# Kernel tuning notes

Hardware: AMD Instinct MI355X
Metric: run time of the kernel (lower is better)

The kernel has to match this reference:

```python
import jax, jax.numpy as jnp
import numpy as np

B, D, G, L = 8, 128, 2048, 24
GF = G // 2 + 1  # rfft bins
EPS = 1e-5


def setup_inputs() -> dict:
    key = jax.random.key(0)
    ks = jax.random.split(key, 6)
    x = jax.random.normal(ks[0], (B, D, G), dtype=jnp.float32)
    Phi_f = jax.random.normal(ks[1], (L, GF), dtype=jnp.float32) * 0.1
    Theta = jax.random.normal(ks[2], (L, D, D), dtype=jnp.float32) * (1.0 / np.sqrt(D))
    ln_gamma = jnp.ones((D,), dtype=jnp.float32)
    ln_beta = jnp.zeros((D,), dtype=jnp.float32)
    fc1_w = jax.random.normal(ks[3], (2 * D, D), dtype=jnp.float32) * (1.0 / np.sqrt(D))
    fc1_b = jnp.zeros((2 * D,), dtype=jnp.float32)
    fc2_w = jax.random.normal(ks[4], (D, 2 * D), dtype=jnp.float32) * (1.0 / np.sqrt(2 * D))
    fc2_b = jnp.zeros((D,), dtype=jnp.float32)
    return {
        'x': x, 'Phi_f': Phi_f, 'Theta': Theta,
        'ln_gamma': ln_gamma, 'ln_beta': ln_beta,
        'fc1_w': fc1_w, 'fc1_b': fc1_b, 'fc2_w': fc2_w, 'fc2_b': fc2_b,
    }


def reference(x, Phi_f, Theta, ln_gamma, ln_beta, fc1_w, fc1_b, fc2_w, fc2_b):
    # x: (B, D, G). LayerNorm over the lifting (channel) dim D.
    mean = jnp.mean(x, axis=1, keepdims=True)
    var = jnp.var(x, axis=1, keepdims=True)
    z = (x - mean) * jax.lax.rsqrt(var + EPS)
    z = z * ln_gamma[None, :, None] + ln_beta[None, :, None]

    # Spectral convolution with each Hilbert filter.
    Xf = jnp.fft.rfft(z, axis=-1)                       # (B, D, GF) complex
    Uf = Xf[:, :, None, :] * jnp.conj(Phi_f)[None, None]  # (B, D, L, GF)
    U = jnp.fft.irfft(Uf, n=G, axis=-1)                 # (B, D, L, G)

    # Per-filter channel mixing then reduction over filters:
    # einsum('bdln,lhd->bhln') followed by sum over l, fused:
    S = jnp.einsum('bdlg,lhd->bhg', U, Theta)           # (B, D, G)

    # Pointwise MLP (Conv1d kernel_size=1 == channel matmul).
    H = jnp.einsum('hd,bdg->bhg', fc1_w, S) + fc1_b[None, :, None]
    H = jax.nn.gelu(H, approximate=False)
    out = jnp.einsum('dh,bhg->bdg', fc2_w, H) + fc2_b[None, :, None]
    return x + out
```

## Files before the change

kernel.cpp:

```cpp
#include <hip/hip_runtime.h>
#include <math.h>


#define B_   8
#define D_   128
#define G_   2048
#define L_   24
#define GF_  1025
#define BD_  1024
#define DD_  16384
#define GQ_  512
#define MC_  512
#define NF4_ 4096

#define PA_CV0 256
#define PA_TT0 322
#define PA_WF0 578
#define PA_WI0 1090
#define PA_END 1602

#define G1_NB  512
#define G1_END 4736

typedef __attribute__((ext_vector_type(8))) short  short8v;
typedef __attribute__((ext_vector_type(4))) float  float4v;

union FU { float f; unsigned int u; };
union V8 { short8v v; ushort u[8]; };
union V4 { uint2 p; ushort u[4]; };

static __device__ __forceinline__ float bf2f(ushort h) {
    FU v; v.u = ((unsigned int)h) << 16; return v.f;
}
static __device__ __forceinline__ ushort f2bf(float f) {
    FU v; v.f = f;
    unsigned int r = v.u + 0x7fffu + ((v.u >> 16) & 1u);
    return (ushort)(r >> 16);
}
static __device__ __forceinline__ void async16(const void* g, void* l) {
    __builtin_amdgcn_global_load_lds(
        (const __attribute__((address_space(1))) void*)g,
        (__attribute__((address_space(3))) void*)l, 16, 0, 0);
}
static __device__ __forceinline__ int is_f32(const unsigned int* graw) {
    return graw[0] == 0x3F800000u;
}
static __device__ __forceinline__ void crow_inv(int c, int& f, int& im) {
    if (c == 0) { f = 0; im = 0; }
    else        { f = (c + 1) >> 1; im = (c + 1) & 1; }
}

__global__ __launch_bounds__(256) void k_pre(
        const void* __restrict__ x_raw,  const void* __restrict__ th_raw,
        const unsigned int* __restrict__ graw, const void* __restrict__ be_raw,
        const void* __restrict__ w1_raw, const void* __restrict__ b1_raw,
        const void* __restrict__ w2_raw, const void* __restrict__ b2_raw,
        ushort* __restrict__ z,  ushort* __restrict__ wf,
        ushort* __restrict__ wi, ushort* __restrict__ thT,
        ushort* __restrict__ w1c, ushort* __restrict__ b1c,
        ushort* __restrict__ w2c, ushort* __restrict__ b2c) {
    __shared__ ushort T[L_][72];
    __shared__ float red[2][256];
    __shared__ float mi[2][64];
    int bid = blockIdx.x, tid = threadIdx.x;

    if (bid < PA_CV0) {
        int fl = is_f32(graw);
        int b  = bid >> 5;
        int g0 = (bid & 31) * 64;
        int gi = tid & 63, dq = tid >> 6;
        int g  = g0 + gi;
        int d0 = dq * 32;
        float vals[32];
        float s = 0.f, ss = 0.f;
        if (fl) {
            const float* xp = (const float*)x_raw + (size_t)(b * D_ + d0) * G_ + g;
            #pragma unroll 8
            for (int d = 0; d < 32; ++d) {
                float v = xp[(size_t)d * G_];
                vals[d] = v; s += v; ss += v * v;
            }
        } else {
            const ushort* xp = (const ushort*)x_raw + (size_t)(b * D_ + d0) * G_ + g;
            #pragma unroll 8
            for (int d = 0; d < 32; ++d) {
                float v = bf2f(xp[(size_t)d * G_]);
                vals[d] = v; s += v; ss += v * v;
            }
        }
        red[0][tid] = s; red[1][tid] = ss;
        __syncthreads();
        if (tid < 64) {
            float S  = red[0][tid] + red[0][tid + 64] + red[0][tid + 128] +
                       red[0][tid + 192];
            float SS = red[1][tid] + red[1][tid + 64] + red[1][tid + 128] +
                       red[1][tid + 192];
            float mean = S * (1.f / D_);
            float var  = SS * (1.f / D_) - mean * mean;
            mi[0][tid] = mean;
            mi[1][tid] = rsqrtf(var + 1e-5f);
        }
        __syncthreads();
        float mean = mi[0][gi], inv = mi[1][gi];
        ushort* zp = z + (size_t)(g & 3) * (BD_ * GQ_) +
                     (size_t)(b * D_ + d0) * GQ_ + (g >> 2);
        if (fl) {
            const float* gp = (const float*)graw + d0;
            const float* bp = (const float*)be_raw + d0;
            #pragma unroll 8
            for (int d = 0; d < 32; ++d) {
                float o = (vals[d] - mean) * inv * gp[d] + bp[d];
                zp[(size_t)d * GQ_] = f2bf(o);
            }
        } else {
            const ushort* gp = (const ushort*)graw + d0;
            const ushort* bp = (const ushort*)be_raw + d0;
            #pragma unroll 8
            for (int d = 0; d < 32; ++d) {
                float o = (vals[d] - mean) * inv * bf2f(gp[d]) + bf2f(bp[d]);
                zp[(size_t)d * GQ_] = f2bf(o);
            }
        }
    } else if (bid < PA_TT0) {
        int fl = is_f32(graw);
        int lb = bid - PA_CV0;
        const void* src; ushort* dst; int n, rel;
        if (lb < 32)       { src = w1_raw; dst = w1c; n = 32768; rel = lb; }
        else if (lb == 32) { src = b1_raw; dst = b1c; n = 256;   rel = 0; }
        else if (lb < 65)  { src = w2_raw; dst = w2c; n = 32768; rel = lb - 33; }
        else               { src = b2_raw; dst = b2c; n = 128;   rel = 0; }
        int i0 = rel * 1024 + tid * 4;
        if (fl) {
            const float* s = (const float*)src;
            #pragma unroll
            for (int j = 0; j < 4; ++j) {
                int k = i0 + j;
                if (k < n) dst[k] = f2bf(s[k]);
            }
        } else {
            const ushort* s = (const ushort*)src;
            #pragma unroll
            for (int j = 0; j < 4; ++j) {
                int k = i0 + j;
                if (k < n) dst[k] = s[k];
            }
        }
    } else if (bid < PA_WF0) {
        int fl = is_f32(graw);
        int hd0 = (bid - PA_TT0) * 64;
        if (tid < 192) {
            int l = tid >> 3, c8 = tid & 7;
            V8 o;
            if (fl) {
                const float* tp = (const float*)th_raw + (size_t)l * DD_ +
                                  hd0 + c8 * 8;
                float4v a0 = *(const float4v*)tp;
                float4v a1 = *(const float4v*)(tp + 4);
                #pragma unroll
                for (int j = 0; j < 4; ++j) {
                    o.u[j] = f2bf(a0[j]); o.u[4 + j] = f2bf(a1[j]);
                }
            } else {
                o.v = *(const short8v*)((const ushort*)th_raw +
                                        (size_t)l * DD_ + hd0 + c8 * 8);
            }
            *(short8v*)&T[l][c8 * 8] = o.v;
        }
        __syncthreads();
        int hdl = tid & 63, part = tid >> 6;
        V8 o;
        #pragma unroll
        for (int j = 0; j < 8; ++j) {
            int l = part * 8 + j;
            o.u[j] = (l < L_) ? T[l][hdl] : (ushort)0;
        }
        *(short8v*)(thT + (size_t)(hd0 + hdl) * 32 + part * 8) = o.v;
    } else if (bid < PA_WI0) {
        int c = bid - PA_WF0;
        if (tid < 128) {
            int f, im; crow_inv(c, f, im);
            int g0 = tid * 4;
            V4 v;
            #pragma unroll
            for (int j = 0; j < 4; ++j) {
                int g = g0 + j;
                int r = (f * g) & (GQ_ - 1);
                float th = (float)r * 1.2271846303085130e-2f;
                v.u[j] = f2bf(im ? -__sinf(th) : __cosf(th));
            }
            *(uint2*)(wf + (size_t)c * GQ_ + g0) = v.p;
        }
    } else {
        int g = bid - PA_WI0;
        for (int ch = tid; ch < MC_ / 8; ch += 256) {
            int c0 = ch * 8;
            V8 v;
            #pragma unroll
            for (int j = 0; j < 8; ++j) {
                int c = c0 + j;
                int f, im; crow_inv(c, f, im);
                float a = (f == 0 || f == GQ_ / 2) ? 4.8828125e-4f
                                                   : 9.765625e-4f;
                int r = (f * g) & (GQ_ - 1);
                float th = (float)r * 1.2271846303085130e-2f;
                v.u[j] = f2bf(im ? -a * __sinf(th) : a * __cosf(th));
            }
            *(short8v*)(wi + (size_t)g * MC_ + c0) = v.v;
        }
    }
}

__global__ __launch_bounds__(256, 4) void k_g1(
        const ushort* __restrict__ wf, const ushort* __restrict__ z,
        ushort* __restrict__ zft,
        const void* __restrict__ phi_raw, const unsigned int* __restrict__ graw,
        const ushort* __restrict__ thT, ushort* __restrict__ M) {
    __shared__ ushort As[2][64 * 64];
    __shared__ ushort Bs[2][64 * 64];
    __shared__ ushort Aph[16][40];
    int bid = blockIdx.x, tid = threadIdx.x;
    int w = tid >> 6, lane = tid & 63;
    int lr = lane & 15, q = lane >> 4;

    if (bid < G1_NB) {
        int m0 = (bid >> 6) * 64;
        int n0 = (bid & 63) * 64;
        int wm = (w & 1) * 32, wn = (w >> 1) * 32;
        int rl = lane >> 3, c8 = (lane & 7) ^ rl;
        int t0 = w * 2, t1 = w * 2 + 1;
        const ushort* gA0 = wf + (size_t)(m0 + t0 * 8 + rl) * GQ_ + c8 * 8;
        const ushort* gA1 = wf + (size_t)(m0 + t1 * 8 + rl) * GQ_ + c8 * 8;
        const ushort* gB0 = z  + (size_t)(n0 + t0 * 8 + rl) * GQ_ + c8 * 8;
        const ushort* gB1 = z  + (size_t)(n0 + t1 * 8 + rl) * GQ_ + c8 * 8;

        float4v acc00 = {0.f,0.f,0.f,0.f}, acc01 = {0.f,0.f,0.f,0.f};
        float4v acc10 = {0.f,0.f,0.f,0.f}, acc11 = {0.f,0.f,0.f,0.f};

        async16(gA0, &As[0][t0 * 512]);
        async16(gA1, &As[0][t1 * 512]);
        async16(gB0, &Bs[0][t0 * 512]);
        async16(gB1, &Bs[0][t1 * 512]);
        __syncthreads();

        int buf = 0;
        for (int k0 = 0; k0 < GQ_; k0 += 64) {
            if (k0 + 64 < GQ_) {
                int nb = buf ^ 1;
                async16(gA0 + k0 + 64, &As[nb][t0 * 512]);
                async16(gA1 + k0 + 64, &As[nb][t1 * 512]);
                async16(gB0 + k0 + 64, &Bs[nb][t0 * 512]);
                async16(gB1 + k0 + 64, &Bs[nb][t1 * 512]);
            }
            const ushort* Ab = &As[buf][0];
            const ushort* Bb = &Bs[buf][0];
            #pragma unroll
            for (int s = 0; s < 2; ++s) {
                int cs = s * 4 + q;
                int ra0 = wm + lr, ra1 = wm + 16 + lr;
                int rb0 = wn + lr, rb1 = wn + 16 + lr;
                short8v a0 = *(const short8v*)(Ab + ra0 * 64 + ((cs ^ (ra0 & 7)) << 3));
                short8v a1 = *(const short8v*)(Ab + ra1 * 64 + ((cs ^ (ra1 & 7)) << 3));
                short8v b0 = *(const short8v*)(Bb + rb0 * 64 + ((cs ^ (rb0 & 7)) << 3));
                short8v b1 = *(const short8v*)(Bb + rb1 * 64 + ((cs ^ (rb1 & 7)) << 3));
                acc00 = __builtin_amdgcn_mfma_f32_16x16x32_bf16(a0, b0, acc00, 0, 0, 0);
                acc01 = __builtin_amdgcn_mfma_f32_16x16x32_bf16(a0, b1, acc01, 0, 0, 0);
                acc10 = __builtin_amdgcn_mfma_f32_16x16x32_bf16(a1, b0, acc10, 0, 0, 0);
                acc11 = __builtin_amdgcn_mfma_f32_16x16x32_bf16(a1, b1, acc11, 0, 0, 0);
            }
            __syncthreads();
            buf ^= 1;
        }

        float4v accs[2][2] = { { acc00, acc01 }, { acc10, acc11 } };
        #pragma unroll
        for (int i = 0; i < 2; ++i)
            #pragma unroll
            for (int j = 0; j < 2; ++j) {
                int col = n0 + wn + j * 16 + lr;
                int row = m0 + wm + i * 16 + q * 4;
                #pragma unroll
                for (int r = 0; r < 4; ++r)
                    zft[(size_t)(row + r) * NF4_ + col] = f2bf(accs[i][j][r]);
            }
    } else {
        int bb  = bid - G1_NB;
        int f0  = (bb >> 6) * 16;
        int hd0 = (bb & 63) * 256;
        int isf = is_f32(graw);
        #pragma unroll
        for (int rep = 0; rep < 2; ++rep) {
            int idx = rep * 256 + tid;
            int fl = idx >> 5, l = idx & 31;
            int f = f0 + fl;
            ushort v = 0;
            if (l < L_ && f < GF_)
                v = isf ? f2bf(((const float*)phi_raw)[(size_t)l * GF_ + f])
                        : ((const ushort*)phi_raw)[(size_t)l * GF_ + f];
            Aph[fl][l] = v;
        }
        __syncthreads();
        short8v a = *(const short8v*)&Aph[lr][q * 8];
        #pragma unroll
        for (int t = 0; t < 4; ++t) {
            int n = hd0 + (w * 4 + t) * 16 + lr;
            short8v b = *(const short8v*)(thT + (size_t)n * 32 + q * 8);
            float4v c = {0.f, 0.f, 0.f, 0.f};
            c = __builtin_amdgcn_mfma_f32_16x16x32_bf16(a, b, c, 0, 0, 0);
            #pragma unroll
            for (int r = 0; r < 4; ++r) {
                int f = f0 + q * 4 + r;
                if (f < GF_) M[(size_t)f * DD_ + n] = f2bf(c[r]);
            }
        }
    }
}

__global__ __launch_bounds__(256, 2) void k_mix3(const ushort* __restrict__ zft,
                                                 const ushort* __restrict__ M,
                                                 ushort* __restrict__ sft) {
    int bx  = blockIdx.x;
    int fp  = bx >> 1;
    int hh  = bx & 1;
    int tid = threadIdx.x;
    int w = tid >> 6, lane = tid & 63;
    int lr = lane & 15, q = lane >> 4;
    int cc = lr >> 3, bb = lr & 7;
    int ntg = hh * 4 + w;

    int rowRe  = (fp == 0) ? 0 : (fp == 256 ? 511 : 2 * fp - 1);
    int rowIm  = (fp == 0 || fp == 256) ? rowRe : 2 * fp;
    bool has_im = (fp != 0) && (fp != 256);

    float a1 = (float)fp * 3.0679615757712823e-3f;
    float C1 = cosf(a1),        S1 = sinf(a1);
    float C2 = cosf(2.f * a1),  S2 = sinf(2.f * a1);
    float C3 = cosf(3.f * a1),  S3 = sinf(3.f * a1);

    float P01 = cc ? -S1 :  C1,  Q01 = cc ?  C1 :  S1;
    float P02 = cc ? -S2 :  C2,  Q02 = cc ?  C2 :  S2;
    float P03 = cc ? -S3 :  C3,  Q03 = cc ?  C3 :  S3;
    float P11 = cc ? -C1 :  S1,  Q11 = cc ? -S1 : -C1;
    float P12 = cc ? -S2 : -C2,  Q12 = cc ?  C2 : -S2;
    float P13 = cc ?  C3 : -S3,  Q13 = cc ?  S3 :  C3;
    float P21 = cc ? -C1 : -S1,  Q21 = cc ? -S1 :  C1;
    float P22 = cc ?  S2 : -C2,  Q22 = cc ? -C2 : -S2;
    float P23 = cc ?  C3 :  S3,  Q23 = cc ?  S3 : -C3;
    float P31 = cc ? -S1 : -C1,  Q31 = cc ?  C1 : -S1;
    float P32 = cc ?  S2 :  C2,  Q32 = cc ? -C2 :  S2;
    float P33 = cc ? -S3 : -C3,  Q33 = cc ?  C3 : -S3;

    const ushort* r0 = zft + (size_t)rowRe * NF4_;
    const ushort* r1 = zft + (size_t)rowIm * NF4_;
    int colb = bb * 128 + q * 8;

    short8v aZ[4][4];
    #pragma unroll
    for (int s = 0; s < 4; ++s) {
        int col = colb + s * 32;
        V8 R0, I0, R1, I1, R2, I2, R3, I3;
        R0.v = *(const short8v*)(r0 + col);
        I0.v = *(const short8v*)(r1 + col);
        R1.v = *(const short8v*)(r0 + 1024 + col);
        I1.v = *(const short8v*)(r1 + 1024 + col);
        R2.v = *(const short8v*)(r0 + 2048 + col);
        I2.v = *(const short8v*)(r1 + 2048 + col);
        R3.v = *(const short8v*)(r0 + 3072 + col);
        I3.v = *(const short8v*)(r1 + 3072 + col);
        if (!has_im) {
            #pragma unroll
            for (int e = 0; e < 8; ++e) {
                I0.u[e] = 0; I1.u[e] = 0; I2.u[e] = 0; I3.u[e] = 0;
            }
        }
        V8 t0, t1, t2, t3;
        #pragma unroll
        for (int e = 0; e < 8; ++e) {
            float x0 = bf2f(R0.u[e]), y0 = bf2f(I0.u[e]);
            float x1 = bf2f(R1.u[e]), y1 = bf2f(I1.u[e]);
            float x2 = bf2f(R2.u[e]), y2 = bf2f(I2.u[e]);
            float x3 = bf2f(R3.u[e]), y3 = bf2f(I3.u[e]);
            float e0p = cc ?  y0 : x0;
            float e0m = cc ? -y0 : x0;
            float z0 = e0p, z1 = e0m, z2 = e0p, z3 = e0m;
            z0 = fmaf(P01, x1, z0); z0 = fmaf(Q01, y1, z0);
            z0 = fmaf(P02, x2, z0); z0 = fmaf(Q02, y2, z0);
            z0 = fmaf(P03, x3, z0); z0 = fmaf(Q03, y3, z0);
            z1 = fmaf(P11, x1, z1); z1 = fmaf(Q11, y1, z1);
            z1 = fmaf(P12, x2, z1); z1 = fmaf(Q12, y2, z1);
            z1 = fmaf(P13, x3, z1); z1 = fmaf(Q13, y3, z1);
            z2 = fmaf(P21, x1, z2); z2 = fmaf(Q21, y1, z2);
            z2 = fmaf(P22, x2, z2); z2 = fmaf(Q22, y2, z2);
            z2 = fmaf(P23, x3, z2); z2 = fmaf(Q23, y3, z2);
            z3 = fmaf(P31, x1, z3); z3 = fmaf(Q31, y1, z3);
            z3 = fmaf(P32, x2, z3); z3 = fmaf(Q32, y2, z3);
            z3 = fmaf(P33, x3, z3); z3 = fmaf(Q33, y3, z3);
            t0.u[e] = f2bf(z0); t1.u[e] = f2bf(z1);
            t2.u[e] = f2bf(z2); t3.u[e] = f2bf(z3);
        }
        aZ[0][s] = t0.v; aZ[1][s] = t1.v; aZ[2][s] = t2.v; aZ[3][s] = t3.v;
    }

    int fk0 = fp, fk1 = 512 - fp, fk2 = 512 + fp, fk3 = 1024 - fp;
    const ushort* Mp[4] = { M + (size_t)fk0 * DD_, M + (size_t)fk1 * DD_,
                            M + (size_t)fk2 * DD_, M + (size_t)fk3 * DD_ };
    float4v acc[4];
    #pragma unroll
    for (int k = 0; k < 4; ++k) {
        float4v c = {0.f, 0.f, 0.f, 0.f};
        #pragma unroll
        for (int s = 0; s < 4; ++s) {
            short8v bfr = *(const short8v*)(Mp[k] + (size_t)(ntg * 16 + lr) * D_ +
                                            s * 32 + q * 8);
            c = __builtin_amdgcn_mfma_f32_16x16x32_bf16(aZ[k][s], bfr, c, 0, 0, 0);
        }
        acc[k] = c;
    }

    #pragma unroll
    for (int e = 0; e < 4; ++e) {
        int p   = q * 4 + e;
        int c2i = p >> 3, cb = p & 7;
        float sg = c2i ? -1.f : 1.f;
        float u0 = acc[0][e], u1 = acc[1][e], u2 = acc[2][e], u3 = acc[3][e];
        float p1 = __shfl_xor(u1, 32);
        float p2 = __shfl_xor(u2, 32);
        float U0 = u0 + u2 + sg * (u1 + u3);
        float U1 = u0 - sg * p2 - sg * u3 - p1;
        float U2 = u0 - u2 + sg * (u3 - u1);
        float U3 = u0 + sg * p2 - sg * u3 + p1;
        float U1p = __shfl_xor(U1, 32);
        float U2p = __shfl_xor(U2, 32);
        float U3p = __shfl_xor(U3, 32);
        float T1 = fmaf(-sg * S1, U1p, C1 * U1);
        float T2 = fmaf(-sg * S2, U2p, C2 * U2);
        float T3 = fmaf(-sg * S3, U3p, C3 * U3);
        int orow = c2i ? rowIm : rowRe;
        if (has_im || c2i == 0) {
            size_t base = (size_t)orow * NF4_ + cb * 128 + ntg * 16 + lr;
            sft[base]          = f2bf(U0);
            sft[base + 1024]   = f2bf(T1);
            sft[base + 2048]   = f2bf(T2);
            sft[base + 3072]   = f2bf(T3);
        }
    }
}

__global__ __launch_bounds__(256, 4) void k_gemm64t(const ushort* __restrict__ A,
                                                    const ushort* __restrict__ Bm,
                                                    ushort* __restrict__ C,
                                                    int K, int lda, int ldb,
                                                    int ldc, int kv) {
    __shared__ ushort As[2][64 * 64];
    __shared__ ushort Bs[2][64 * 64];
    int tid = threadIdx.x;
    int m0 = blockIdx.x * 64, n0 = blockIdx.y * 64;
    int w = tid >> 6, lane = tid & 63;
    int lr = lane & 15, q = lane >> 4;
    int wm = (w & 1) * 32, wn = (w >> 1) * 32;

    int rl = lane >> 3, c8 = (lane & 7) ^ rl;
    int t0 = w * 2, t1 = w * 2 + 1;
    const ushort* gA0 = A + (size_t)(m0 + t0 * 8 + rl) * lda + c8 * 8;
    const ushort* gA1 = A + (size_t)(m0 + t1 * 8 + rl) * lda + c8 * 8;

    int br = tid >> 2;
    int bc = tid & 3;

    float4v acc00 = {0.f,0.f,0.f,0.f}, acc01 = {0.f,0.f,0.f,0.f};
    float4v acc10 = {0.f,0.f,0.f,0.f}, acc11 = {0.f,0.f,0.f,0.f};

    async16(gA0, &As[0][t0 * 512]);
    async16(gA1, &As[0][t1 * 512]);
    {
        V8 u0, u1;
        if (br < kv) {
            const ushort* gb = Bm + (size_t)br * ldb + n0 + bc * 16;
            u0.v = *(const short8v*)gb;
            u1.v = *(const short8v*)(gb + 8);
        } else {
            #pragma unroll
            for (int j = 0; j < 8; ++j) { u0.u[j] = 0; u1.u[j] = 0; }
        }
        #pragma unroll
        for (int j = 0; j < 8; ++j) {
            int n = bc * 16 + j;
            Bs[0][n * 64 + ((((br >> 3) ^ (n & 7)) << 3) | (br & 7))] = u0.u[j];
        }
        #pragma unroll
        for (int j = 0; j < 8; ++j) {
            int n = bc * 16 + 8 + j;
            Bs[0][n * 64 + ((((br >> 3) ^ (n & 7)) << 3) | (br & 7))] = u1.u[j];
        }
    }
    __syncthreads();

    int buf = 0;
    for (int k0 = 0; k0 < K; k0 += 64) {
        V8 u0, u1;
        bool more = (k0 + 64 < K);
        if (more) {
            int nb = buf ^ 1;
            async16(gA0 + k0 + 64, &As[nb][t0 * 512]);
            async16(gA1 + k0 + 64, &As[nb][t1 * 512]);
            int kr = k0 + 64 + br;
            if (kr < kv) {
                const ushort* gb = Bm + (size_t)kr * ldb + n0 + bc * 16;
                u0.v = *(const short8v*)gb;
                u1.v = *(const short8v*)(gb + 8);
            } else {
                #pragma unroll
                for (int j = 0; j < 8; ++j) { u0.u[j] = 0; u1.u[j] = 0; }
            }
        }
        const ushort* Ab = &As[buf][0];
        const ushort* Bb = &Bs[buf][0];
        #pragma unroll
        for (int s = 0; s < 2; ++s) {
            int cs = s * 4 + q;
            int ra0 = wm + lr, ra1 = wm + 16 + lr;
            int rb0 = wn + lr, rb1 = wn + 16 + lr;
            short8v a0 = *(const short8v*)(Ab + ra0 * 64 + ((cs ^ (ra0 & 7)) << 3));
            short8v a1 = *(const short8v*)(Ab + ra1 * 64 + ((cs ^ (ra1 & 7)) << 3));
            short8v b0 = *(const short8v*)(Bb + rb0 * 64 + ((cs ^ (rb0 & 7)) << 3));
            short8v b1 = *(const short8v*)(Bb + rb1 * 64 + ((cs ^ (rb1 & 7)) << 3));
            acc00 = __builtin_amdgcn_mfma_f32_16x16x32_bf16(a0, b0, acc00, 0, 0, 0);
            acc01 = __builtin_amdgcn_mfma_f32_16x16x32_bf16(a0, b1, acc01, 0, 0, 0);
            acc10 = __builtin_amdgcn_mfma_f32_16x16x32_bf16(a1, b0, acc10, 0, 0, 0);
            acc11 = __builtin_amdgcn_mfma_f32_16x16x32_bf16(a1, b1, acc11, 0, 0, 0);
        }
        __syncthreads();
        if (more) {
            int nb = buf ^ 1;
            #pragma unroll
            for (int j = 0; j < 8; ++j) {
                int n = bc * 16 + j;
                Bs[nb][n * 64 + ((((br >> 3) ^ (n & 7)) << 3) | (br & 7))] = u0.u[j];
            }
            #pragma unroll
            for (int j = 0; j < 8; ++j) {
                int n = bc * 16 + 8 + j;
                Bs[nb][n * 64 + ((((br >> 3) ^ (n & 7)) << 3) | (br & 7))] = u1.u[j];
            }
        }
        __syncthreads();
        buf ^= 1;
    }

    float4v accs[2][2] = { { acc00, acc01 }, { acc10, acc11 } };
    #pragma unroll
    for (int i = 0; i < 2; ++i)
        #pragma unroll
        for (int j = 0; j < 2; ++j) {
            int col = n0 + wn + j * 16 + lr;
            int row = m0 + wm + i * 16 + q * 4;
            #pragma unroll
            for (int r = 0; r < 4; ++r)
                C[(size_t)(row + r) * ldc + col] = f2bf(accs[i][j][r]);
        }
}

#define MLPG 32
__global__ __launch_bounds__(256, 2) void k_mlp3(const ushort* __restrict__ ST,
                                                 const void* __restrict__ x0,
                                                 const ushort* __restrict__ w1,
                                                 const ushort* __restrict__ b1,
                                                 const ushort* __restrict__ w2,
                                                 const ushort* __restrict__ b2,
                                                 const unsigned int* __restrict__ graw,
                                                 void* __restrict__ outv) {
    __shared__ ushort Sb[MLPG][136];
    __shared__ ushort Hb[MLPG][264];
    __shared__ float  Ob[128][36];
    int g0 = blockIdx.x * MLPG, b = blockIdx.y;
    int tid = threadIdx.x;
    {
        int col = tid >> 3, seg = tid & 7;
        int g = g0 + col;
        const ushort* sp = ST + (size_t)(g >> 2) * NF4_ + (g & 3) * BD_ +
                           b * D_ + seg * 16;
        short8v s0 = *(const short8v*)(sp);
        short8v s1 = *(const short8v*)(sp + 8);
        *(short8v*)&Sb[col][seg * 16]     = s0;
        *(short8v*)&Sb[col][seg * 16 + 8] = s1;
    }
    __syncthreads();
    int w = tid >> 6, lane = tid & 63;
    int lr = lane & 15, q = lane >> 4;
    int nt = w & 1, mh = w >> 1;

    {
        float4v acc[8];
        #pragma unroll
        for (int i = 0; i < 8; ++i) { float4v zz = {0.f,0.f,0.f,0.f}; acc[i] = zz; }
        #pragma unroll
        for (int ks = 0; ks < 4; ++ks) {
            short8v bf = *(const short8v*)&Sb[nt * 16 + lr][ks * 32 + q * 8];
            #pragma unroll
            for (int i = 0; i < 8; ++i) {
                int mt = mh * 8 + i;
                short8v af = *(const short8v*)(w1 + (size_t)(mt * 16 + lr) * D_ +
                                               ks * 32 + q * 8);
                acc[i] = __builtin_amdgcn_mfma_f32_16x16x32_bf16(af, bf, acc[i], 0, 0, 0);
            }
        }
        #pragma unroll
        for (int i = 0; i < 8; ++i) {
            int h0 = (mh * 8 + i) * 16 + q * 4;
            V4 hv;
            #pragma unroll
            for (int r = 0; r < 4; ++r) {
                float v = acc[i][r] + bf2f(b1[h0 + r]);
                v = 0.5f * v * (1.f + erff(v * 0.70710678118f));
                hv.u[r] = f2bf(v);
            }
            *(uint2*)&Hb[nt * 16 + lr][h0] = hv.p;
        }
    }
    __syncthreads();
    {
        float4v acc2[4];
        #pragma unroll
        for (int j = 0; j < 4; ++j) { float4v zz = {0.f,0.f,0.f,0.f}; acc2[j] = zz; }
        #pragma unroll
        for (int ks = 0; ks < 8; ++ks) {
            short8v bf = *(const short8v*)&Hb[nt * 16 + lr][ks * 32 + q * 8];
            #pragma unroll
            for (int j = 0; j < 4; ++j) {
                int mt2 = mh * 4 + j;
                short8v af = *(const short8v*)(w2 + (size_t)(mt2 * 16 + lr) * (2 * D_) +
                                               ks * 32 + q * 8);
                acc2[j] = __builtin_amdgcn_mfma_f32_16x16x32_bf16(af, bf, acc2[j], 0, 0, 0);
            }
        }
        int col = nt * 16 + lr;
        #pragma unroll
        for (int j = 0; j < 4; ++j) {
            int d0 = (mh * 4 + j) * 16 + q * 4;
            #pragma unroll
            for (int r = 0; r < 4; ++r)
                Ob[d0 + r][col] = acc2[j][r] + bf2f(b2[d0 + r]);
        }
    }
    __syncthreads();
    {
        int fl = is_f32(graw);
        if (fl) {
            #pragma unroll
            for (int p = 0; p < 4; ++p) {
                int idx = p * 256 + tid;
                int d = idx >> 3, c4 = (idx & 7) * 4;
                float4v o = *(const float4v*)&Ob[d][c4];
                size_t gidx = ((size_t)(b * D_ + d)) * G_ + g0 + c4;
                float4v xv = *(const float4v*)((const float*)x0 + gidx);
                float4v ov;
                #pragma unroll
                for (int k = 0; k < 4; ++k) ov[k] = o[k] + xv[k];
                *(float4v*)((float*)outv + gidx) = ov;
            }
        } else {
            #pragma unroll
            for (int p = 0; p < 4; ++p) {
                int idx = p * 256 + tid;
                int d = idx >> 3, c4 = (idx & 7) * 4;
                float4v o = *(const float4v*)&Ob[d][c4];
                size_t gidx = ((size_t)(b * D_ + d)) * G_ + g0 + c4;
                V4 xv; xv.p = *(const uint2*)((const ushort*)x0 + gidx);
                V4 ov;
                #pragma unroll
                for (int k = 0; k < 4; ++k) ov.u[k] = f2bf(o[k] + bf2f(xv.u[k]));
                *(uint2*)((ushort*)outv + gidx) = ov.p;
            }
        }
    }
}

extern "C" void kernel_launch(void* const* d_in, const int* in_sizes, int n_in,
                              void* d_out, int out_size, void* d_ws, size_t ws_size,
                              hipStream_t stream) {
    char* base = (char*)d_ws;
    ushort* z    = (ushort*)(base);
    ushort* wf   = (ushort*)(base + 4194304);
    ushort* sft  = (ushort*)(base);
    ushort* zft  = (ushort*)(base + 13107200);
    ushort* st   = (ushort*)(base + 13107200);
    ushort* w1c  = (ushort*)(base + 27050048);
    ushort* b1c  = (ushort*)(base + 27115584);
    ushort* w2c  = (ushort*)(base + 27116096);
    ushort* b2c  = (ushort*)(base + 27181632);
    ushort* Mm   = (ushort*)(base + 27182592);
    ushort* wi   = (ushort*)(base + 60769792);
    ushort* thT  = (ushort*)(base + 69420544);

    const unsigned int* graw = (const unsigned int*)d_in[3];

    k_pre    <<<dim3(PA_END), 256, 0, stream>>>(
        d_in[0], d_in[2], graw, d_in[4], d_in[5], d_in[6], d_in[7], d_in[8],
        z, wf, wi, thT, w1c, b1c, w2c, b2c);
    k_g1     <<<dim3(G1_END), 256, 0, stream>>>(wf, z, zft, d_in[1], graw,
                                                thT, Mm);
    k_mix3   <<<dim3(514), 256, 0, stream>>>(zft, Mm, sft);
    k_gemm64t<<<dim3(GQ_ / 64, NF4_ / 64), 256, 0, stream>>>(
        wi, sft, st, MC_, MC_, NF4_, NF4_, MC_);
    k_mlp3   <<<dim3(G_ / MLPG, B_), 256, 0, stream>>>(st, d_in[0], w1c, b1c,
                                                       w2c, b2c, graw, d_out);
}
```

Measured before the change: 158.0 us.

## Store spectral mix output K-contiguous so GEMM loads B tiles asynchronously

The mixing kernel now writes its bf16 output transposed, with the reduction dimension contiguous per output column. The GEMM can then fetch B tiles with the same async global-to-LDS copies used for A. This removes the register round-trip, the element-wise swizzled LDS scatter, one barrier per K step and the kv bounds check. In exchange, the mixing kernel's stores become strided 2-byte writes spread across rows, which may coalesce poorly.

```diff
diff --git a/kernel.cpp b/kernel.cpp
--- a/kernel.cpp
+++ b/kernel.cpp
@@ -436,11 +436,12 @@
         float T3 = fmaf(-sg * S3, U3p, C3 * U3);
         int orow = c2i ? rowIm : rowRe;
         if (has_im || c2i == 0) {
-            size_t base = (size_t)orow * NF4_ + cb * 128 + ntg * 16 + lr;
-            sft[base]          = f2bf(U0);
-            sft[base + 1024]   = f2bf(T1);
-            sft[base + 2048]   = f2bf(T2);
-            sft[base + 3072]   = f2bf(T3);
+            int ncol = cb * 128 + ntg * 16 + lr;
+            ushort* sp = sft + (size_t)ncol * MC_ + orow;
+            sp[0]                  = f2bf(U0);
+            sp[(size_t)1024 * MC_] = f2bf(T1);
+            sp[(size_t)2048 * MC_] = f2bf(T2);
+            sp[(size_t)3072 * MC_] = f2bf(T3);
         }
     }
 }
@@ -449,7 +450,7 @@
                                                     const ushort* __restrict__ Bm,
                                                     ushort* __restrict__ C,
                                                     int K, int lda, int ldb,
-                                                    int ldc, int kv) {
+                                                    int ldc) {
     __shared__ ushort As[2][64 * 64];
     __shared__ ushort Bs[2][64 * 64];
     int tid = threadIdx.x;
@@ -460,57 +461,28 @@
 
     int rl = lane >> 3, c8 = (lane & 7) ^ rl;
     int t0 = w * 2, t1 = w * 2 + 1;
-    const ushort* gA0 = A + (size_t)(m0 + t0 * 8 + rl) * lda + c8 * 8;
-    const ushort* gA1 = A + (size_t)(m0 + t1 * 8 + rl) * lda + c8 * 8;
-
-    int br = tid >> 2;
-    int bc = tid & 3;
+    const ushort* gA0 = A  + (size_t)(m0 + t0 * 8 + rl) * lda + c8 * 8;
+    const ushort* gA1 = A  + (size_t)(m0 + t1 * 8 + rl) * lda + c8 * 8;
+    const ushort* gB0 = Bm + (size_t)(n0 + t0 * 8 + rl) * ldb + c8 * 8;
+    const ushort* gB1 = Bm + (size_t)(n0 + t1 * 8 + rl) * ldb + c8 * 8;
 
     float4v acc00 = {0.f,0.f,0.f,0.f}, acc01 = {0.f,0.f,0.f,0.f};
     float4v acc10 = {0.f,0.f,0.f,0.f}, acc11 = {0.f,0.f,0.f,0.f};
 
     async16(gA0, &As[0][t0 * 512]);
     async16(gA1, &As[0][t1 * 512]);
-    {
-        V8 u0, u1;
-        if (br < kv) {
-            const ushort* gb = Bm + (size_t)br * ldb + n0 + bc * 16;
-            u0.v = *(const short8v*)gb;
-            u1.v = *(const short8v*)(gb + 8);
-        } else {
-            #pragma unroll
-            for (int j = 0; j < 8; ++j) { u0.u[j] = 0; u1.u[j] = 0; }
-        }
-        #pragma unroll
-        for (int j = 0; j < 8; ++j) {
-            int n = bc * 16 + j;
-            Bs[0][n * 64 + ((((br >> 3) ^ (n & 7)) << 3) | (br & 7))] = u0.u[j];
-        }
-        #pragma unroll
-        for (int j = 0; j < 8; ++j) {
-            int n = bc * 16 + 8 + j;
-            Bs[0][n * 64 + ((((br >> 3) ^ (n & 7)) << 3) | (br & 7))] = u1.u[j];
-        }
-    }
+    async16(gB0, &Bs[0][t0 * 512]);
+    async16(gB1, &Bs[0][t1 * 512]);
     __syncthreads();
 
     int buf = 0;
     for (int k0 = 0; k0 < K; k0 += 64) {
-        V8 u0, u1;
-        bool more = (k0 + 64 < K);
-        if (more) {
+        if (k0 + 64 < K) {
             int nb = buf ^ 1;
             async16(gA0 + k0 + 64, &As[nb][t0 * 512]);
             async16(gA1 + k0 + 64, &As[nb][t1 * 512]);
-            int kr = k0 + 64 + br;
-            if (kr < kv) {
-                const ushort* gb = Bm + (size_t)kr * ldb + n0 + bc * 16;
-                u0.v = *(const short8v*)gb;
-                u1.v = *(const short8v*)(gb + 8);
-            } else {
-                #pragma unroll
-                for (int j = 0; j < 8; ++j) { u0.u[j] = 0; u1.u[j] = 0; }
-            }
+            async16(gB0 + k0 + 64, &Bs[nb][t0 * 512]);
+            async16(gB1 + k0 + 64, &Bs[nb][t1 * 512]);
         }
         const ushort* Ab = &As[buf][0];
         const ushort* Bb = &Bs[buf][0];
@@ -527,20 +499,6 @@
             acc01 = __builtin_amdgcn_mfma_f32_16x16x32_bf16(a0, b1, acc01, 0, 0, 0);
             acc10 = __builtin_amdgcn_mfma_f32_16x16x32_bf16(a1, b0, acc10, 0, 0, 0);
             acc11 = __builtin_amdgcn_mfma_f32_16x16x32_bf16(a1, b1, acc11, 0, 0, 0);
-        }
-        __syncthreads();
-        if (more) {
-            int nb = buf ^ 1;
-            #pragma unroll
-            for (int j = 0; j < 8; ++j) {
-                int n = bc * 16 + j;
-                Bs[nb][n * 64 + ((((br >> 3) ^ (n & 7)) << 3) | (br & 7))] = u0.u[j];
-            }
-            #pragma unroll
-            for (int j = 0; j < 8; ++j) {
-                int n = bc * 16 + 8 + j;
-                Bs[nb][n * 64 + ((((br >> 3) ^ (n & 7)) << 3) | (br & 7))] = u1.u[j];
-            }
         }
         __syncthreads();
         buf ^= 1;
@@ -700,7 +658,7 @@
                                                 thT, Mm);
     k_mix3   <<<dim3(514), 256, 0, stream>>>(zft, Mm, sft);
     k_gemm64t<<<dim3(GQ_ / 64, NF4_ / 64), 256, 0, stream>>>(
-        wi, sft, st, MC_, MC_, NF4_, NF4_, MC_);
+        wi, sft, st, MC_, MC_, MC_, NF4_);
     k_mlp3   <<<dim3(G_ / MLPG, B_), 256, 0, stream>>>(st, d_in[0], w1c, b1c,
                                                        w2c, b2c, graw, d_out);
 }
```

Measured after the change: 160.7 us. About the same (+1.7%).
